# Kernel optimization log

Measured on AMD Instinct MI355X. Metric: run time of the kernel, lower is better.

Reference implementation:

```python
import jax, jax.numpy as jnp
import numpy as np

B = 2048      # env batch (graphs)
A = 8         # agents per graph (fully connected)
N = B * A     # total nodes
DIN = 192     # raw obs dim
HD = 256      # h_dim (base MLP)
MD = 256      # mem_dim (GRU)
GD = 128      # gnn_dim (per-head GATv2 out, concat=False -> head mean)
H = 4         # GAT heads
NA = 20       # n_actions
ED = 3        # edge_dim


def setup_inputs() -> dict:
    key = jax.random.key(0)
    ks = jax.random.split(key, 16)
    # fully-connected directed graph per group of A agents, no self loops
    s, d = np.meshgrid(np.arange(A), np.arange(A), indexing='ij')
    mask = s != d
    s = s[mask]; d = d[mask]                     # [A*(A-1)]
    off = (np.arange(B) * A)[:, None]
    src = (off + s[None, :]).reshape(-1)
    dst = (off + d[None, :]).reshape(-1)
    edge_index = jnp.asarray(np.stack([src, dst]), dtype=jnp.int32)  # [2, E]
    E = src.shape[0]
    p = lambda k, sh: jax.random.normal(ks[k], sh, jnp.float32) * 0.02
    return {
        'inputs': jax.random.normal(ks[0], (N, DIN), jnp.float32),
        'hidden_states': jax.random.normal(ks[1], (N, MD), jnp.float32) * 0.1,
        'edge_index': edge_index,
        'edge_attr': jax.random.uniform(ks[2], (E, ED), jnp.float32),
        # base MLP (2 layers: Linear+ReLU+LayerNorm)
        'W1': p(3, (DIN, HD)), 'b1': jnp.zeros(HD), 'g1': jnp.ones(HD), 'be1': jnp.zeros(HD),
        'W2': p(4, (HD, HD)),  'b2': jnp.zeros(HD), 'g2': jnp.ones(HD), 'be2': jnp.zeros(HD),
        # GRUCell
        'Wih': p(5, (3 * MD, HD)), 'Whh': p(6, (3 * MD, MD)),
        'bih': jnp.zeros(3 * MD), 'bhh': jnp.zeros(3 * MD),
        # GATv2Conv (edge_dim=3, heads=4, concat=False, residual)
        'Wl': p(7, (MD, H * GD)), 'bl': jnp.zeros(H * GD),
        'Wr': p(8, (MD, H * GD)), 'br': jnp.zeros(H * GD),
        'att': p(9, (H, GD)),
        'We': p(10, (ED, H * GD)),
        'Wres': p(11, (MD, GD)),
        'bg': jnp.zeros(GD),
        # head: LayerNorm + Linear
        'lng': jnp.ones(GD), 'lnb': jnp.zeros(GD),
        'Wout': p(12, (GD, NA)), 'bout': jnp.zeros(NA),
    }


def _ln(x, g, b):
    mu = jnp.mean(x, -1, keepdims=True)
    xc = x - mu
    v = jnp.mean(xc * xc, -1, keepdims=True)
    return xc * jax.lax.rsqrt(v + 1e-5) * g + b


def _fwd(inputs, hidden_states, edge_attr, edge_index,
         W1, b1, g1, be1, W2, b2, g2, be2,
         Wih, Whh, bih, bhh,
         Wl, bl, Wr, br, att, We, Wres, bg,
         lng, lnb, Wout, bout):
    src, dst = edge_index[0], edge_index[1]
    # ---- base MLP encode ----
    x = _ln(jax.nn.relu(inputs @ W1 + b1), g1, be1)
    x = _ln(jax.nn.relu(x @ W2 + b2), g2, be2)          # [N, HD]
    # ---- SimpleConv(aggr='mean', combine_root='self_loop') ----
    s = jax.ops.segment_sum(x[src], dst, num_segments=N) + x
    deg = jax.ops.segment_sum(jnp.ones(src.shape[0], x.dtype), dst, num_segments=N) + 1.0
    x = s / deg[:, None]                                 # [N, HD]
    # ---- GRUCell ----
    gi = x @ Wih.T + bih
    gh = hidden_states @ Whh.T + bhh
    ir, iz, inn = jnp.split(gi, 3, -1)
    hr, hz, hn = jnp.split(gh, 3, -1)
    r = jax.nn.sigmoid(ir + hr)
    z = jax.nn.sigmoid(iz + hz)
    n = jnp.tanh(inn + r * hn)
    h = (1.0 - z) * n + z * hidden_states                # [N, MD]
    # ---- GATv2Conv (add self loops, edge_attr fill='mean') ----
    loop = jnp.arange(N, dtype=src.dtype)
    sf = jnp.concatenate([src, loop])
    df = jnp.concatenate([dst, loop])
    ea = jnp.concatenate([edge_attr, jnp.broadcast_to(edge_attr.mean(0), (N, ED))], 0)
    xl = (h @ Wl + bl).reshape(N, H, GD)
    xr = (h @ Wr + br).reshape(N, H, GD)
    m = xl[sf] + xr[df] + (ea @ We).reshape(-1, H, GD)   # [Ef, H, GD]
    m = jnp.where(m > 0, m, 0.2 * m)                     # leaky_relu(0.2)
    logits = jnp.einsum('ehc,hc->eh', m, att)            # [Ef, H]
    mx = jax.ops.segment_max(logits, df, num_segments=N)
    ex = jnp.exp(logits - mx[df])
    den = jax.ops.segment_sum(ex, df, num_segments=N)
    alpha = ex / (den[df] + 1e-16)                       # segment softmax
    out = jax.ops.segment_sum(xl[sf] * alpha[..., None], df, num_segments=N)
    out = out.mean(1) + h @ Wres + bg                    # head mean + residual + bias
    zg = jax.nn.relu(out)                                # [N, GD]
    # ---- action head ----
    q = _ln(zg, lng, lnb) @ Wout + bout                  # [N, NA]
    return q, h


def reference(inputs, hidden_states, edge_index, edge_attr,
              W1, b1, g1, be1, W2, b2, g2, be2,
              Wih, Whh, bih, bhh,
              Wl, bl, Wr, br, att, We, Wres, bg,
              lng, lnb, Wout, bout):
    return _fwd(inputs, hidden_states, edge_attr, edge_index,
                W1, b1, g1, be1, W2, b2, g2, be2,
                Wih, Whh, bih, bhh,
                Wl, bl, Wr, br, att, We, Wres, bg,
                lng, lnb, Wout, bout)
```

## Files before the change

### kernel.cpp

```cpp
#include <hip/hip_runtime.h>
#include <hip/hip_bf16.h>

constexpr int NB  = 2048;
constexpr int AG  = 8;
constexpr int NN  = NB * AG;
constexpr int DIN = 192;
constexpr int HD  = 256;
constexpr int MD  = 256;
constexpr int GD  = 128;
constexpr int NA  = 20;
constexpr int NE  = NB * AG * (AG - 1);

typedef __attribute__((ext_vector_type(8))) short bfrag8;
typedef __attribute__((ext_vector_type(4))) short sfrag4;
typedef __attribute__((ext_vector_type(4))) float f32x4;

#define MFMA16(a, b, c) __builtin_amdgcn_mfma_f32_16x16x32_bf16((a), (b), (c), 0, 0, 0)

#define GLOAD_LDS16(g, l) __builtin_amdgcn_global_load_lds(                  \
    (const __attribute__((address_space(1))) void*)(g),                      \
    (__attribute__((address_space(3))) void*)(l), 16, 0, 0)

__device__ __forceinline__ float bf2f(__hip_bfloat16 x) { return __bfloat162float(x); }
__device__ __forceinline__ __hip_bfloat16 f2bf(float x) { return __float2bfloat16(x); }
__device__ __forceinline__ short f2bs(float x) {
    __hip_bfloat16 b = __float2bfloat16(x);
    return *reinterpret_cast<short*>(&b);
}
__device__ __forceinline__ bfrag8 ldf(const __hip_bfloat16* p) { return *(const bfrag8*)p; }
__device__ __forceinline__ bfrag8 ldf32(const float* p) {
    const f32x4 a = *(const f32x4*)p;
    const f32x4 b = *(const f32x4*)(p + 4);
    bfrag8 r;
    r[0] = f2bs(a[0]); r[1] = f2bs(a[1]); r[2] = f2bs(a[2]); r[3] = f2bs(a[3]);
    r[4] = f2bs(b[0]); r[5] = f2bs(b[1]); r[6] = f2bs(b[2]); r[7] = f2bs(b[3]);
    return r;
}
__device__ __forceinline__ float sigmf(float x) { return 1.f / (1.f + __expf(-x)); }
__device__ __forceinline__ float blo(unsigned u) { return __uint_as_float(u << 16); }
__device__ __forceinline__ float bhi(unsigned u) { return __uint_as_float(u & 0xffff0000u); }

__global__ __launch_bounds__(256) void k_prep(
    const float* __restrict__ W1, const float* __restrict__ W2,
    const float* __restrict__ Wih, const float* __restrict__ Whh,
    const float* __restrict__ Wl, const float* __restrict__ bl,
    const float* __restrict__ Wr, const float* __restrict__ br,
    const float* __restrict__ Wres, const float* __restrict__ Wout,
    const float* __restrict__ ea,
    __hip_bfloat16* __restrict__ W1T, __hip_bfloat16* __restrict__ W2T,
    __hip_bfloat16* __restrict__ WihB, __hip_bfloat16* __restrict__ WhhB,
    __hip_bfloat16* __restrict__ WcatT, float* __restrict__ WoutTf,
    float* __restrict__ bcat, float* __restrict__ ea_partials)
{
    __shared__ float sw[4][3];
    const int tid = threadIdx.x;
    if (blockIdx.x >= 3151) {
        const int b = blockIdx.x - 3151;
        float a0 = 0.f, a1 = 0.f, a2 = 0.f;
#pragma unroll
        for (int k = 0; k < 7; k++) {
            int e = b * 1792 + k * 256 + tid;
            a0 += ea[e * 3 + 0];
            a1 += ea[e * 3 + 1];
            a2 += ea[e * 3 + 2];
        }
#pragma unroll
        for (int off = 1; off < 64; off <<= 1) {
            a0 += __shfl_xor(a0, off); a1 += __shfl_xor(a1, off); a2 += __shfl_xor(a2, off);
        }
        if ((tid & 63) == 0) { sw[tid >> 6][0] = a0; sw[tid >> 6][1] = a1; sw[tid >> 6][2] = a2; }
        __syncthreads();
        if (tid == 0) {
            ea_partials[b * 3 + 0] = sw[0][0] + sw[1][0] + sw[2][0] + sw[3][0];
            ea_partials[b * 3 + 1] = sw[0][1] + sw[1][1] + sw[2][1] + sw[3][1];
            ea_partials[b * 3 + 2] = sw[0][2] + sw[1][2] + sw[2][2] + sw[3][2];
        }
        return;
    }
    int i = blockIdx.x * 256 + tid;
    if (i < 49152) { int o = i / 192, c = i % 192; W1T[i] = f2bf(W1[c * 256 + o]); return; }
    i -= 49152;
    if (i < 65536) { int o = i >> 8, c = i & 255; W2T[i] = f2bf(W2[c * 256 + o]); return; }
    i -= 65536;
    if (i < 196608) { WihB[i] = f2bf(Wih[i]); return; }
    i -= 196608;
    if (i < 196608) { WhhB[i] = f2bf(Whh[i]); return; }
    i -= 196608;
    if (i < 294912) {
        int o = i >> 8, c = i & 255;
        float v;
        if (o < 512)       v = Wl[c * 512 + o];
        else if (o < 1024) v = Wr[c * 512 + (o - 512)];
        else               v = Wres[c * 128 + (o - 1024)];
        WcatT[i] = f2bf(v); return;
    }
    i -= 294912;
    if (i < 2560) { int o = i >> 7, c = i & 127; WoutTf[i] = Wout[c * 20 + o]; return; }
    i -= 2560;
    if (i < 1152) {
        float v = 0.f;
        if (i < 512) v = bl[i]; else if (i < 1024) v = br[i - 512];
        bcat[i] = v;
    }
}

__global__ __launch_bounds__(256) void k_encode(
    const float* __restrict__ in,
    const __hip_bfloat16* __restrict__ W1T,
    const float* __restrict__ b1, const float* __restrict__ g1, const float* __restrict__ be1,
    const __hip_bfloat16* __restrict__ W2T,
    const float* __restrict__ b2, const float* __restrict__ g2, const float* __restrict__ be2,
    __hip_bfloat16* __restrict__ xm)
{
    __shared__ float sf[16][257];
    __shared__ alignas(16) __hip_bfloat16 sb[16][264];
    const int tid = threadIdx.x;
    const int lane = tid & 63, w = tid >> 6;
    const int r = lane & 15, q = lane >> 4;
    const int m0 = blockIdx.x * 16;

    {
        bfrag8 af[6];
        const float* ap = in + (size_t)(m0 + r) * DIN + q * 8;
#pragma unroll
        for (int kb = 0; kb < 6; kb++) af[kb] = ldf32(ap + kb * 32);
#pragma unroll
        for (int i = 0; i < 4; i++) {
            int t = w * 4 + i;
            const __hip_bfloat16* wp = W1T + (size_t)(t * 16 + r) * DIN + q * 8;
            bfrag8 bf[6];
#pragma unroll
            for (int kb = 0; kb < 6; kb++) bf[kb] = ldf(wp + kb * 32);
            f32x4 acc = (f32x4){0.f, 0.f, 0.f, 0.f};
#pragma unroll
            for (int kb = 0; kb < 6; kb++) acc = MFMA16(af[kb], bf[kb], acc);
            int col = t * 16 + r;
            float bias = b1[col];
#pragma unroll
            for (int reg = 0; reg < 4; reg++)
                sf[q * 4 + reg][col] = fmaxf(acc[reg] + bias, 0.f);
        }
    }
    __syncthreads();
    {
        int rowi = tid >> 4, c16 = tid & 15;
        float vals[16]; float s = 0.f, s2 = 0.f;
#pragma unroll
        for (int j = 0; j < 16; j++) { float v = sf[rowi][c16 + 16 * j]; vals[j] = v; s += v; s2 += v * v; }
#pragma unroll
        for (int off = 1; off < 16; off <<= 1) { s += __shfl_xor(s, off); s2 += __shfl_xor(s2, off); }
        float mean = s * (1.f / HD);
        float var = fmaxf(s2 * (1.f / HD) - mean * mean, 0.f);
        float rs = rsqrtf(var + 1e-5f);
#pragma unroll
        for (int j = 0; j < 16; j++) {
            int col = c16 + 16 * j;
            sb[rowi][col] = f2bf((vals[j] - mean) * rs * g1[col] + be1[col]);
        }
    }
    __syncthreads();

    {
        bfrag8 af[8];
        const __hip_bfloat16* ap = &sb[r][0];
#pragma unroll
        for (int kb = 0; kb < 8; kb++) af[kb] = ldf(ap + kb * 32 + q * 8);
        float outv[4][4];
#pragma unroll
        for (int i = 0; i < 4; i++) {
            int t = w * 4 + i;
            const __hip_bfloat16* wp = W2T + (size_t)(t * 16 + r) * HD + q * 8;
            bfrag8 bf[8];
#pragma unroll
            for (int kb = 0; kb < 8; kb++) bf[kb] = ldf(wp + kb * 32);
            f32x4 acc = (f32x4){0.f, 0.f, 0.f, 0.f};
#pragma unroll
            for (int kb = 0; kb < 8; kb++) acc = MFMA16(af[kb], bf[kb], acc);
#pragma unroll
            for (int reg = 0; reg < 4; reg++) outv[i][reg] = acc[reg];
        }
        __syncthreads();
#pragma unroll
        for (int i = 0; i < 4; i++) {
            int col = (w * 4 + i) * 16 + r;
            float bias = b2[col];
#pragma unroll
            for (int reg = 0; reg < 4; reg++)
                sf[q * 4 + reg][col] = fmaxf(outv[i][reg] + bias, 0.f);
        }
    }
    __syncthreads();
    {
        int rowi = tid >> 4, c16 = tid & 15;
        float vals[16]; float s = 0.f, s2 = 0.f;
#pragma unroll
        for (int j = 0; j < 16; j++) { float v = sf[rowi][c16 + 16 * j]; vals[j] = v; s += v; s2 += v * v; }
#pragma unroll
        for (int off = 1; off < 16; off <<= 1) { s += __shfl_xor(s, off); s2 += __shfl_xor(s2, off); }
        float mean = s * (1.f / HD);
        float var = fmaxf(s2 * (1.f / HD) - mean * mean, 0.f);
        float rs = rsqrtf(var + 1e-5f);
#pragma unroll
        for (int j = 0; j < 16; j++) {
            int col = c16 + 16 * j;
            sb[rowi][col] = f2bf((vals[j] - mean) * rs * g2[col] + be2[col]);
        }
    }
    __syncthreads();
    {
        int col = tid;
        float a0 = 0.f, a1 = 0.f;
#pragma unroll
        for (int i = 0; i < 8; i++) { a0 += bf2f(sb[i][col]); a1 += bf2f(sb[8 + i][col]); }
        xm[(size_t)(2 * blockIdx.x) * HD + col] = f2bf(a0 * 0.125f);
        xm[(size_t)(2 * blockIdx.x + 1) * HD + col] = f2bf(a1 * 0.125f);
    }
}

__global__ __launch_bounds__(256, 2) void k_gruG(
    const float* __restrict__ hprev,
    const __hip_bfloat16* __restrict__ WhhB,
    const float* __restrict__ bhh,
    const __hip_bfloat16* __restrict__ xm,
    const __hip_bfloat16* __restrict__ WihB,
    const float* __restrict__ bih,
    float* __restrict__ hout)
{
    __shared__ alignas(16) float sgi[16][200];
    const int tid = threadIdx.x;
    const int lane = tid & 63, w = tid >> 6;
    const int r = lane & 15, q = lane >> 4;
    const int bswz = (blockIdx.x & 7) * 64 + (blockIdx.x >> 3);
    const int m0 = (bswz >> 2) * 128;
    const int cg = (bswz & 3) * 64;

    {
        const int g0 = m0 >> 3;
        bfrag8 axm[8];
        const __hip_bfloat16* ap = xm + (size_t)(g0 + r) * MD + q * 8;
#pragma unroll
        for (int kb = 0; kb < 8; kb++) axm[kb] = ldf(ap + kb * 32);
#pragma unroll
        for (int i = 0; i < 3; i++) {
            const int n = w * 3 + i;
            const int gate = n >> 2, nj = n & 3;
            const int colG = gate * 256 + cg + nj * 16 + r;
            const __hip_bfloat16* wp = WihB + (size_t)colG * MD + q * 8;
            bfrag8 bf[8];
#pragma unroll
            for (int kb = 0; kb < 8; kb++) bf[kb] = ldf(wp + kb * 32);
            f32x4 acg = (f32x4){0.f, 0.f, 0.f, 0.f};
#pragma unroll
            for (int kb = 0; kb < 8; kb++) acg = MFMA16(axm[kb], bf[kb], acg);
            const float bias = bih[colG];
#pragma unroll
            for (int reg = 0; reg < 4; reg++)
                sgi[q * 4 + reg][n * 16 + r] = acg[reg] + bias;
        }
    }

    bfrag8 afr[2][8];
#pragma unroll
    for (int t = 0; t < 2; t++) {
        const float* ap = hprev + (size_t)(m0 + (w * 2 + t) * 16 + r) * MD + q * 8;
#pragma unroll
        for (int kb = 0; kb < 8; kb++) afr[t][kb] = ldf32(ap + kb * 32);
    }
    __syncthreads();

    f32x4 acc[2][12];
#pragma unroll
    for (int t = 0; t < 2; t++)
#pragma unroll
        for (int n = 0; n < 12; n++) acc[t][n] = (f32x4){0.f, 0.f, 0.f, 0.f};

#pragma unroll
    for (int kb = 0; kb < 8; kb++) {
        bfrag8 bfB[12];
#pragma unroll
        for (int g = 0; g < 3; g++)
#pragma unroll
            for (int nj = 0; nj < 4; nj++)
                bfB[g * 4 + nj] = ldf(WhhB + (size_t)(g * 256 + cg + nj * 16 + r) * MD
                                      + kb * 32 + q * 8);
#pragma unroll
        for (int t = 0; t < 2; t++)
#pragma unroll
            for (int n = 0; n < 12; n++)
                acc[t][n] = MFMA16(bfB[n], afr[t][kb], acc[t][n]);
    }

#pragma unroll
    for (int t = 0; t < 2; t++) {
        int node = m0 + (w * 2 + t) * 16 + r;
        int gl = ((w * 2 + t) * 16 + r) >> 3;
#pragma unroll
        for (int nj = 0; nj < 4; nj++) {
            int c = cg + nj * 16 + q * 4;
            int ci = nj * 16 + q * 4;
            f32x4 gR = *(const f32x4*)&sgi[gl][ci];
            f32x4 gZ = *(const f32x4*)&sgi[gl][64 + ci];
            f32x4 gN = *(const f32x4*)&sgi[gl][128 + ci];
            f32x4 bR = *(const f32x4*)&bhh[c];
            f32x4 bZ = *(const f32x4*)&bhh[256 + c];
            f32x4 bN = *(const f32x4*)&bhh[512 + c];
            f32x4 hp = *(const f32x4*)&hprev[(size_t)node * MD + c];
            f32x4 hv;
#pragma unroll
            for (int reg = 0; reg < 4; reg++) {
                float rr = sigmf(gR[reg] + acc[t][0 + nj][reg] + bR[reg]);
                float zz = sigmf(gZ[reg] + acc[t][4 + nj][reg] + bZ[reg]);
                float nn = tanhf(gN[reg] + rr * (acc[t][8 + nj][reg] + bN[reg]));
                hv[reg] = (1.f - zz) * nn + zz * hp[reg];
            }
            *(f32x4*)&hout[(size_t)node * MD + c] = hv;
        }
    }
}

__global__ __launch_bounds__(256, 2) void k_xlr(
    const float* __restrict__ h,
    const __hip_bfloat16* __restrict__ WcatT,
    const float* __restrict__ bcat,
    __hip_bfloat16* __restrict__ xlr)
{
    __shared__ alignas(16) __hip_bfloat16 sB[128 * 64];
    const int tid = threadIdx.x;
    const int lane = tid & 63, w = tid >> 6;
    const int r = lane & 15, q = lane >> 4;
    const int wm = w >> 1, wn = w & 1;

    const int lin = (blockIdx.x & 7) * 144 + (blockIdx.x >> 3);
    const int m0 = (lin / 9) * 128;
    const int nb = (lin % 9) * 128;

    const int srow = tid >> 3;
    const int sch  = (tid & 7) ^ (srow & 7);

    f32x4 acc[4][4];
#pragma unroll
    for (int am = 0; am < 4; am++)
#pragma unroll
        for (int bn = 0; bn < 4; bn++) acc[am][bn] = (f32x4){0.f, 0.f, 0.f, 0.f};

    for (int kt = 0; kt < 4; ++kt) {
        if (kt) __syncthreads();
#pragma unroll
        for (int i = 0; i < 4; ++i) {
            const __hip_bfloat16* gp = WcatT + (size_t)(nb + i * 32 + srow) * 256
                                       + kt * 64 + sch * 8;
            GLOAD_LDS16(gp, &sB[i * 2048 + tid * 8]);
        }
        __syncthreads();

#pragma unroll
        for (int kk = 0; kk < 2; ++kk) {
            bfrag8 af[4], bf[4];
#pragma unroll
            for (int am = 0; am < 4; ++am)
                af[am] = ldf32(h + (size_t)(m0 + wm * 64 + am * 16 + r) * MD
                               + kt * 64 + kk * 32 + q * 8);
#pragma unroll
            for (int bn = 0; bn < 4; ++bn) {
                const int R = wn * 64 + bn * 16 + r;
                const int c = (kk * 4 + q) ^ (R & 7);
                bf[bn] = *(const bfrag8*)&sB[R * 64 + c * 8];
            }
#pragma unroll
            for (int am = 0; am < 4; ++am)
#pragma unroll
                for (int bn = 0; bn < 4; ++bn)
                    acc[am][bn] = MFMA16(bf[bn], af[am], acc[am][bn]);
        }
    }

#pragma unroll
    for (int bn = 0; bn < 4; ++bn) {
        const int fb = nb + wn * 64 + bn * 16 + q * 4;
        const f32x4 bv = *(const f32x4*)&bcat[fb];
#pragma unroll
        for (int am = 0; am < 4; ++am) {
            const int node = m0 + wm * 64 + am * 16 + r;
            sfrag4 pk;
#pragma unroll
            for (int reg = 0; reg < 4; reg++) pk[reg] = f2bs(acc[am][bn][reg] + bv[reg]);
            *(sfrag4*)&xlr[(size_t)node * 1152 + fb] = pk;
        }
    }
}

__global__ __launch_bounds__(128, 4) void k_gat(
    const __hip_bfloat16* __restrict__ xlr,
    const float* __restrict__ ea,
    const float* __restrict__ ea_partials,
    const float* __restrict__ att,
    const float* __restrict__ We,
    const float* __restrict__ bg,
    const float* __restrict__ lng, const float* __restrict__ lnb,
    const float* __restrict__ WoutTf,
    const float* __restrict__ bout,
    float* __restrict__ qout)
{
    __shared__ alignas(16) char smem_raw[8 * 1160 * 2];
    __shared__ float slog[4][8][8];
    __shared__ float smean[4];
    __hip_bfloat16 (*sx)[1160] = (__hip_bfloat16 (*)[1160])smem_raw;
    float (*szg)[136] = (float (*)[136])smem_raw;
    const int tid = threadIdx.x;
    const int lane = tid & 63, w = tid >> 6;
    const int g = blockIdx.x;
    const int m0 = g * 8;

    if (tid < 3) {
        float s = 0.f;
        for (int i = 0; i < 64; i++) s += ea_partials[i * 3 + tid];
        smean[tid] = s * (1.f / NE);
    }
#pragma unroll
    for (int k = 0; k < 9; k++) {
        int idx = tid + k * 128;
        int row = idx / 144, off = (idx % 144) * 8;
        *(uint4*)&sx[row][off] = *(const uint4*)&xlr[(size_t)(m0 + row) * 1152 + off];
    }

    const int sL = lane & 7, dL = lane >> 3;
    float e0 = 0.f, e1 = 0.f, e2 = 0.f;
    if (sL != dL) {
        int eidx = sL * 7 + dL - (dL > sL ? 1 : 0);
        const float* ep = ea + (size_t)(g * 56 + eidx) * 3;
        e0 = ep[0]; e1 = ep[1]; e2 = ep[2];
    }
    __syncthreads();
    if (sL == dL) { e0 = smean[0]; e1 = smean[1]; e2 = smean[2]; }

    {
        const __hip_bfloat16* xlrow = &sx[sL][0];
        const __hip_bfloat16* xrrow = &sx[dL][512];
#pragma unroll
        for (int t = 0; t < 2; t++) {
            const int hh = w * 2 + t;
            const int woff = __builtin_amdgcn_readfirstlane(hh * 128);
            const float* attp = att + woff;
            const float* w0p = We + woff;
            const float* w1p = We + 512 + woff;
            const float* w2p = We + 1024 + woff;
            const __hip_bfloat16* xlp = xlrow + hh * 128;
            const __hip_bfloat16* xrp = xrrow + hh * 128;
            float p0 = 0.f, p1 = 0.f;
#pragma unroll 4
            for (int cb = 0; cb < 16; cb++) {
                const uint4 uxl = *(const uint4*)&xlp[cb * 8];
                const uint4 uxr = *(const uint4*)&xrp[cb * 8];
                const f32x4 a0  = *(const f32x4*)&attp[cb * 8];
                const f32x4 a1  = *(const f32x4*)&attp[cb * 8 + 4];
                const f32x4 w00 = *(const f32x4*)&w0p[cb * 8];
                const f32x4 w01 = *(const f32x4*)&w0p[cb * 8 + 4];
                const f32x4 w10 = *(const f32x4*)&w1p[cb * 8];
                const f32x4 w11 = *(const f32x4*)&w1p[cb * 8 + 4];
                const f32x4 w20 = *(const f32x4*)&w2p[cb * 8];
                const f32x4 w21 = *(const f32x4*)&w2p[cb * 8 + 4];
                float mm;
#define CH1(XL, XR, WA, WB, WC, AT, ACC)                                          \
                mm = fmaf(e2, (WC), fmaf(e1, (WB), fmaf(e0, (WA), (XL)))) + (XR); \
                mm = fmaxf(mm, 0.2f * mm); ACC = fmaf(mm, (AT), ACC);
                CH1(blo(uxl.x), blo(uxr.x), w00[0], w10[0], w20[0], a0[0], p0)
                CH1(bhi(uxl.x), bhi(uxr.x), w00[1], w10[1], w20[1], a0[1], p1)
                CH1(blo(uxl.y), blo(uxr.y), w00[2], w10[2], w20[2], a0[2], p0)
                CH1(bhi(uxl.y), bhi(uxr.y), w00[3], w10[3], w20[3], a0[3], p1)
                CH1(blo(uxl.z), blo(uxr.z), w01[0], w11[0], w21[0], a1[0], p0)
                CH1(bhi(uxl.z), bhi(uxr.z), w01[1], w11[1], w21[1], a1[1], p1)
                CH1(blo(uxl.w), blo(uxr.w), w01[2], w11[2], w21[2], a1[2], p0)
                CH1(bhi(uxl.w), bhi(uxr.w), w01[3], w11[3], w21[3], a1[3], p1)
#undef CH1
            }
            float p = p0 + p1;
            float mx = fmaxf(p, __shfl_xor(p, 1));
            mx = fmaxf(mx, __shfl_xor(mx, 2));
            mx = fmaxf(mx, __shfl_xor(mx, 4));
            float exv = __expf(p - mx);
            float den = exv + __shfl_xor(exv, 1);
            den += __shfl_xor(den, 2);
            den += __shfl_xor(den, 4);
            ((float*)&slog[hh][0][0])[lane] = exv / (den + 1e-16f);
        }
    }
    __syncthreads();

    {
        const int d = tid >> 4, cb = (tid & 15) * 8;
        float out[8] = {0.f, 0.f, 0.f, 0.f, 0.f, 0.f, 0.f, 0.f};
#pragma unroll
        for (int h = 0; h < 4; h++) {
#pragma unroll
            for (int s = 0; s < 8; s++) {
                const float al = slog[h][d][s];
                const uint4 u = *(const uint4*)&sx[s][h * 128 + cb];
                out[0] = fmaf(al, blo(u.x), out[0]);
                out[1] = fmaf(al, bhi(u.x), out[1]);
                out[2] = fmaf(al, blo(u.y), out[2]);
                out[3] = fmaf(al, bhi(u.y), out[3]);
                out[4] = fmaf(al, blo(u.z), out[4]);
                out[5] = fmaf(al, bhi(u.z), out[5]);
                out[6] = fmaf(al, blo(u.w), out[6]);
                out[7] = fmaf(al, bhi(u.w), out[7]);
            }
        }
        const uint4 ur = *(const uint4*)&sx[d][1024 + cb];
        const f32x4 bg0 = *(const f32x4*)&bg[cb];
        const f32x4 bg1 = *(const f32x4*)&bg[cb + 4];
        f32x4 ov0, ov1;
        ov0[0] = fmaxf(out[0] * 0.25f + blo(ur.x) + bg0[0], 0.f);
        ov0[1] = fmaxf(out[1] * 0.25f + bhi(ur.x) + bg0[1], 0.f);
        ov0[2] = fmaxf(out[2] * 0.25f + blo(ur.y) + bg0[2], 0.f);
        ov0[3] = fmaxf(out[3] * 0.25f + bhi(ur.y) + bg0[3], 0.f);
        ov1[0] = fmaxf(out[4] * 0.25f + blo(ur.z) + bg1[0], 0.f);
        ov1[1] = fmaxf(out[5] * 0.25f + bhi(ur.z) + bg1[1], 0.f);
        ov1[2] = fmaxf(out[6] * 0.25f + blo(ur.w) + bg1[2], 0.f);
        ov1[3] = fmaxf(out[7] * 0.25f + bhi(ur.w) + bg1[3], 0.f);
        __syncthreads();
        *(f32x4*)&szg[d][cb]     = ov0;
        *(f32x4*)&szg[d][cb + 4] = ov1;
    }
    __syncthreads();

    {
        int row = tid >> 4, j = tid & 15;
        float v[8]; float s = 0.f, s2 = 0.f;
#pragma unroll
        for (int cj = 0; cj < 8; cj++) { v[cj] = szg[row][j + 16 * cj]; s += v[cj]; s2 += v[cj] * v[cj]; }
#pragma unroll
        for (int off = 1; off < 16; off <<= 1) { s += __shfl_xor(s, off); s2 += __shfl_xor(s2, off); }
        float mean = s * (1.f / GD);
        float var = fmaxf(s2 * (1.f / GD) - mean * mean, 0.f);
        float rs = rsqrtf(var + 1e-5f);
#pragma unroll
        for (int cj = 0; cj < 8; cj++) {
            int c = j + 16 * cj;
            szg[row][c] = (v[cj] - mean) * rs * lng[c] + lnb[c];
        }
    }
    __syncthreads();

    {
        int row = tid >> 4, j = tid & 15;
        for (int jj = j; jj < NA; jj += 16) {
            float a = bout[jj];
            const float* wo = WoutTf + jj * 128;
#pragma unroll
            for (int c4 = 0; c4 < 32; c4++) {
                f32x4 z = *(const f32x4*)&szg[row][c4 * 4];
                const f32x4 wv = *(const f32x4*)&wo[c4 * 4];
                a = fmaf(z[0], wv[0], a); a = fmaf(z[1], wv[1], a);
                a = fmaf(z[2], wv[2], a); a = fmaf(z[3], wv[3], a);
            }
            qout[(size_t)(m0 + row) * NA + jj] = a;
        }
    }
}

extern "C" void kernel_launch(void* const* d_in, const int* in_sizes, int n_in,
                              void* d_out, int out_size, void* d_ws, size_t ws_size,
                              hipStream_t stream) {
    const float* inp   = (const float*)d_in[0];
    const float* hid   = (const float*)d_in[1];
    const float* eatt  = (const float*)d_in[3];
    const float* W1    = (const float*)d_in[4];
    const float* b1    = (const float*)d_in[5];
    const float* g1    = (const float*)d_in[6];
    const float* be1   = (const float*)d_in[7];
    const float* W2    = (const float*)d_in[8];
    const float* b2    = (const float*)d_in[9];
    const float* g2    = (const float*)d_in[10];
    const float* be2   = (const float*)d_in[11];
    const float* Wih   = (const float*)d_in[12];
    const float* Whh   = (const float*)d_in[13];
    const float* bih   = (const float*)d_in[14];
    const float* bhh   = (const float*)d_in[15];
    const float* Wl    = (const float*)d_in[16];
    const float* bl    = (const float*)d_in[17];
    const float* Wr    = (const float*)d_in[18];
    const float* br    = (const float*)d_in[19];
    const float* att   = (const float*)d_in[20];
    const float* We    = (const float*)d_in[21];
    const float* Wres  = (const float*)d_in[22];
    const float* bg    = (const float*)d_in[23];
    const float* lng   = (const float*)d_in[24];
    const float* lnb   = (const float*)d_in[25];
    const float* Wout  = (const float*)d_in[26];
    const float* bout  = (const float*)d_in[27];

    float* qout = (float*)d_out;
    float* hout = (float*)d_out + (size_t)NN * NA;

    char* ws = (char*)d_ws;
    float*           ea_partials = (float*)ws;
    __hip_bfloat16*  xm    = (__hip_bfloat16*)(ws + 2048);
    __hip_bfloat16*  W1T   = (__hip_bfloat16*)(ws + 7342080);
    __hip_bfloat16*  W2T   = (__hip_bfloat16*)(ws + 7440384);
    __hip_bfloat16*  WihB  = (__hip_bfloat16*)(ws + 7571456);
    __hip_bfloat16*  WhhB  = (__hip_bfloat16*)(ws + 7964672);
    __hip_bfloat16*  WcatT = (__hip_bfloat16*)(ws + 8357888);
    float*           bcat  = (float*)(ws + 8947712);
    float*           WoutTf= (float*)(ws + 8952320);
    __hip_bfloat16*  xlr   = (__hip_bfloat16*)(ws + 8962560);

    k_prep<<<3215, 256, 0, stream>>>(W1, W2, Wih, Whh, Wl, bl, Wr, br, Wres, Wout, eatt,
                                     W1T, W2T, WihB, WhhB, WcatT, WoutTf, bcat, ea_partials);
    k_encode<<<NN / 16, 256, 0, stream>>>(inp, W1T, b1, g1, be1, W2T, b2, g2, be2, xm);
    k_gruG<<<512, 256, 0, stream>>>(hid, WhhB, bhh, xm, WihB, bih, hout);
    k_xlr<<<1152, 256, 0, stream>>>(hout, WcatT, bcat, xlr);
    k_gat<<<NB, 128, 0, stream>>>(xlr, eatt, ea_partials, att, We, bg,
                                  lng, lnb, WoutTf, bout, qout);
}
```

Measured before the change: 310.4 us.

## Restructure xlr GEMM into single-wave 64x64 tiles loading operands directly

The xlr projection GEMM moves from 256-thread blocks with 128x128 tiles and an LDS-staged weight tile to 64-thread single-wave blocks computing 64x64 tiles. Each wave now reads both the fp32 hidden state and the bf16 weights straight from global memory into registers, with no shared memory and no barriers. The grid grows fourfold and the block-index swizzle is adjusted to match. This removes LDS staging and synchronisation overhead and raises block-level parallelism, but it gives up LDS reuse of the weights across waves, so global/L2 traffic per FLOP goes up.

Measured after the change: 320.8 us. 1.03x slower.

```diff
diff --git a/kernel.cpp b/kernel.cpp
--- a/kernel.cpp
+++ b/kernel.cpp
@@ -16,10 +16,6 @@
 typedef __attribute__((ext_vector_type(4))) float f32x4;
 
 #define MFMA16(a, b, c) __builtin_amdgcn_mfma_f32_16x16x32_bf16((a), (b), (c), 0, 0, 0)
-
-#define GLOAD_LDS16(g, l) __builtin_amdgcn_global_load_lds(                  \
-    (const __attribute__((address_space(1))) void*)(g),                      \
-    (__attribute__((address_space(3))) void*)(l), 16, 0, 0)
 
 __device__ __forceinline__ float bf2f(__hip_bfloat16 x) { return __bfloat162float(x); }
 __device__ __forceinline__ __hip_bfloat16 f2bf(float x) { return __float2bfloat16(x); }
@@ -318,24 +314,21 @@
     }
 }
 
-__global__ __launch_bounds__(256, 2) void k_xlr(
+__global__ __launch_bounds__(64, 4) void k_xlr(
     const float* __restrict__ h,
     const __hip_bfloat16* __restrict__ WcatT,
     const float* __restrict__ bcat,
     __hip_bfloat16* __restrict__ xlr)
 {
-    __shared__ alignas(16) __hip_bfloat16 sB[128 * 64];
-    const int tid = threadIdx.x;
-    const int lane = tid & 63, w = tid >> 6;
+    const int lane = threadIdx.x;
     const int r = lane & 15, q = lane >> 4;
-    const int wm = w >> 1, wn = w & 1;
-
-    const int lin = (blockIdx.x & 7) * 144 + (blockIdx.x >> 3);
-    const int m0 = (lin / 9) * 128;
-    const int nb = (lin % 9) * 128;
-
-    const int srow = tid >> 3;
-    const int sch  = (tid & 7) ^ (srow & 7);
+
+    const int lin = ((int)blockIdx.x & 7) * 576 + ((int)blockIdx.x >> 3);
+    const int m0 = (lin / 18) * 64;
+    const int nb = (lin % 18) * 64;
+
+    const float* hbase = h + (size_t)(m0 + r) * MD + q * 8;
+    const __hip_bfloat16* wbase = WcatT + (size_t)(nb + r) * MD + q * 8;
 
     f32x4 acc[4][4];
 #pragma unroll
@@ -343,44 +336,29 @@
 #pragma unroll
         for (int bn = 0; bn < 4; bn++) acc[am][bn] = (f32x4){0.f, 0.f, 0.f, 0.f};
 
-    for (int kt = 0; kt < 4; ++kt) {
-        if (kt) __syncthreads();
-#pragma unroll
-        for (int i = 0; i < 4; ++i) {
-            const __hip_bfloat16* gp = WcatT + (size_t)(nb + i * 32 + srow) * 256
-                                       + kt * 64 + sch * 8;
-            GLOAD_LDS16(gp, &sB[i * 2048 + tid * 8]);
-        }
-        __syncthreads();
-
-#pragma unroll
-        for (int kk = 0; kk < 2; ++kk) {
-            bfrag8 af[4], bf[4];
-#pragma unroll
-            for (int am = 0; am < 4; ++am)
-                af[am] = ldf32(h + (size_t)(m0 + wm * 64 + am * 16 + r) * MD
-                               + kt * 64 + kk * 32 + q * 8);
-#pragma unroll
-            for (int bn = 0; bn < 4; ++bn) {
-                const int R = wn * 64 + bn * 16 + r;
-                const int c = (kk * 4 + q) ^ (R & 7);
-                bf[bn] = *(const bfrag8*)&sB[R * 64 + c * 8];
-            }
-#pragma unroll
-            for (int am = 0; am < 4; ++am)
-#pragma unroll
-                for (int bn = 0; bn < 4; ++bn)
-                    acc[am][bn] = MFMA16(bf[bn], af[am], acc[am][bn]);
-        }
+#pragma unroll
+    for (int kb = 0; kb < 8; ++kb) {
+        bfrag8 af[4], bf[4];
+#pragma unroll
+        for (int am = 0; am < 4; ++am)
+            af[am] = ldf32(hbase + (size_t)(am * 16) * MD + kb * 32);
+#pragma unroll
+        for (int bn = 0; bn < 4; ++bn)
+            bf[bn] = ldf(wbase + (size_t)(bn * 16) * MD + kb * 32);
+#pragma unroll
+        for (int am = 0; am < 4; ++am)
+#pragma unroll
+            for (int bn = 0; bn < 4; ++bn)
+                acc[am][bn] = MFMA16(bf[bn], af[am], acc[am][bn]);
     }
 
 #pragma unroll
     for (int bn = 0; bn < 4; ++bn) {
-        const int fb = nb + wn * 64 + bn * 16 + q * 4;
+        const int fb = nb + bn * 16 + q * 4;
         const f32x4 bv = *(const f32x4*)&bcat[fb];
 #pragma unroll
         for (int am = 0; am < 4; ++am) {
-            const int node = m0 + wm * 64 + am * 16 + r;
+            const int node = m0 + am * 16 + r;
             sfrag4 pk;
 #pragma unroll
             for (int reg = 0; reg < 4; reg++) pk[reg] = f2bs(acc[am][bn][reg] + bv[reg]);
@@ -608,7 +586,7 @@
                                      W1T, W2T, WihB, WhhB, WcatT, WoutTf, bcat, ea_partials);
     k_encode<<<NN / 16, 256, 0, stream>>>(inp, W1T, b1, g1, be1, W2T, b2, g2, be2, xm);
     k_gruG<<<512, 256, 0, stream>>>(hid, WhhB, bhh, xm, WihB, bih, hout);
-    k_xlr<<<1152, 256, 0, stream>>>(hout, WcatT, bcat, xlr);
+    k_xlr<<<4608, 64, 0, stream>>>(hout, WcatT, bcat, xlr);
     k_gat<<<NB, 128, 0, stream>>>(xlr, eatt, ea_partials, att, We, bg,
                                   lng, lnb, WoutTf, bout, qout);
 }
```
